# Kernel tuning notes

Measured on AMD Instinct MI355X. Metric: run time of the kernel, lower is better.

## Reference

```python
import jax, jax.numpy as jnp
import numpy as np

E = 256          # embedding_dim
IN = E + 1       # input feature dim (embedding_dim + 1)
B = 128          # batch
N = 1027         # nodes: 1 source + 1024 candidates + 1 destination + 1 depot
REWIRE_P = 0.1


def setup_inputs() -> dict:
    key = jax.random.key(0)
    ks = jax.random.split(key, 16)
    scale = 1.0 / np.sqrt(IN)

    def lin_w(k):
        return jax.random.normal(k, (E, IN), dtype=jnp.float32) * scale

    def lin_b(k):
        return jax.random.normal(k, (E,), dtype=jnp.float32) * scale

    # sparse small-world rewiring weights: nc scalar writes -> one scatter
    nc = int(IN * E * REWIRE_P)  # 6579
    rows = jax.random.randint(ks[10], (nc,), 0, E)
    cols = jax.random.randint(ks[11], (nc,), 0, IN)
    vals = jax.random.normal(ks[12], (nc,), dtype=jnp.float32) * 0.01
    W_rand = jnp.zeros((E, IN), dtype=jnp.float32).at[rows, cols].set(vals)

    return {
        "solutions": jax.random.normal(ks[0], (B, N, IN), dtype=jnp.float32),
        "W_src": lin_w(ks[1]), "b_src": lin_b(ks[2]),
        "W_dst": lin_w(ks[3]), "b_dst": lin_b(ks[4]),
        "W_dep": lin_w(ks[5]), "b_dep": lin_b(ks[6]),
        "W_cand": lin_w(ks[7]), "b_cand": lin_b(ks[8]),
        "W_reg": lin_w(ks[9]), "b_reg": lin_b(ks[13]),
        "W_rand": W_rand,
        "integration_weight": jnp.float32(0.3),
    }


def reference(solutions, W_src, b_src, W_dst, b_dst, W_dep, b_dep,
              W_cand, b_cand, W_reg, b_reg, W_rand, integration_weight):
    # slice node groups: [B,1,IN], [B,N-3,IN], [B,1,IN], [B,1,IN]
    src = solutions[:, :1, :]
    cand = solutions[:, 1:-2, :]
    dst = solutions[:, -2:-1, :]
    dep = solutions[:, -1:, :]

    def lin(x, W, b):
        return jnp.einsum('bnd,ed->bne', x, W) + b

    def sw(x):
        # SmallWorldLayer: regular linear + 0.1 * sparse random matmul
        return lin(x, W_reg, b_reg) + 0.1 * jnp.einsum('bnd,ed->bne', x, W_rand)

    alpha = jax.nn.sigmoid(integration_weight)

    def mix(emb, sw_out):
        return (1.0 - alpha) * emb + alpha * sw_out

    source_emb = mix(lin(src, W_src, b_src), sw(src))
    candidates_emb = mix(lin(cand, W_cand, b_cand), sw(cand))
    destination_emb = mix(lin(dst, W_dst, b_dst), sw(dst))
    depot_emb = mix(lin(dep, W_dep, b_dep), sw(dep))
    return (source_emb, candidates_emb, destination_emb, depot_emb)
```

## Files before the change

kernel.cpp:

```cpp
#include <hip/hip_runtime.h>
#include <hip/hip_bf16.h>

typedef __bf16 bf16x8 __attribute__((ext_vector_type(8)));
typedef __bf16 bf16x4 __attribute__((ext_vector_type(4)));
typedef float  f32x4  __attribute__((ext_vector_type(4)));
typedef float  f32x4u __attribute__((ext_vector_type(4), aligned(4)));

#define BATCH 128
#define NSOL  1027
#define IND   257
#define EMB   256
#define OUT_SRC  0ULL
#define OUT_CAND 32768ULL
#define OUT_DST  33587200ULL
#define OUT_DEP  33619968ULL

#define WFRAG_OFF 0
#define BEFF_OFF  524288
#define W256_OFF  528384

#define XST_B      528
#define X256_OFF_B 16896
#define BUF_B      17024

__global__ __launch_bounds__(256) void swne_prep(
    const float* __restrict__ Wsrc, const float* __restrict__ bsrc,
    const float* __restrict__ Wdst, const float* __restrict__ bdst,
    const float* __restrict__ Wdep, const float* __restrict__ bdep,
    const float* __restrict__ Wcand, const float* __restrict__ bcand,
    const float* __restrict__ Wreg, const float* __restrict__ breg,
    const float* __restrict__ Wrand, const float* __restrict__ iw,
    char* __restrict__ ws)
{
    const float a  = 1.0f / (1.0f + expf(-iw[0]));
    const float ca = 1.0f - a;
    const float sa = 0.1f * a;

    const float* Ws[4] = {Wsrc, Wcand, Wdst, Wdep};
    const float* Bs[4] = {bsrc, bcand, bdst, bdep};

    const int gid = blockIdx.x * 256 + threadIdx.x;
    const int gsz = gridDim.x * 256;

    float* beff = (float*)(ws + BEFF_OFF);
    float* w256 = (float*)(ws + W256_OFF);
    for (int i = gid; i < 4 * EMB; i += gsz) {
        int seg = i >> 8, e = i & 255;
        beff[i] = ca * Bs[seg][e] + a * breg[e];
        int si = e * IND + 256;
        w256[i] = ca * Ws[seg][si] + a * Wreg[si] + sa * Wrand[si];
    }

    __bf16* wfr = (__bf16*)(ws + WFRAG_OFF);
    for (int i = gid; i < 4 * 65536; i += gsz) {
        int seg  = i >> 16;
        int rem  = i & 65535;
        int kk   = rem >> 13;
        int rem2 = rem & 8191;
        int cg   = rem2 >> 9;
        int rem3 = rem2 & 511;
        int l    = rem3 >> 3;
        int j    = rem3 & 7;
        int e = cg * 16 + (l & 15);
        int k = kk * 32 + (l >> 4) * 8 + j;
        int si = e * IND + k;
        wfr[i] = (__bf16)(ca * Ws[seg][si] + a * Wreg[si] + sa * Wrand[si]);
    }
}

__global__ __launch_bounds__(256, 8) void swne_main(const float* __restrict__ sol,
                                                    const char* __restrict__ ws,
                                                    float* __restrict__ out)
{
    __shared__ __align__(16) char smem[BUF_B];
    const int tid = threadIdx.x, bid = blockIdx.x;
    const int lane = tid & 63, wave = tid >> 6;
    const int rl = lane & 15, grp = lane >> 4;

    const float* xbase; size_t xstr; float* obase; int seg;
    if (bid < 4096) {
        const int bb = bid >> 5, t = bid & 31;
        seg   = 1;
        xbase = sol + ((size_t)bb * NSOL + 1 + t * 32) * IND;
        xstr  = IND;
        obase = out + OUT_CAND + ((size_t)bb * 1024 + t * 32) * 256;
    } else {
        const int e = bid - 4096;
        const int s3 = e >> 2, tt = e & 3;
        seg = (s3 == 0) ? 0 : (s3 == 1 ? 2 : 3);
        const int nrow = (s3 == 0) ? 0 : (s3 == 1 ? 1025 : 1026);
        const size_t outb = (s3 == 0) ? OUT_SRC : (s3 == 1 ? OUT_DST : OUT_DEP);
        xbase = sol + ((size_t)(tt * 32) * NSOL + nrow) * IND;
        xstr  = (size_t)NSOL * IND;
        obase = out + outb + (size_t)(tt * 32) * 256;
    }

    #pragma unroll
    for (int rr = 0; rr < 8; ++rr) {
        const int r = wave * 8 + rr;
        f32x4u v = *((const f32x4u*)(xbase + (size_t)r * xstr) + lane);
        bf16x4 h;
        h[0] = (__bf16)v[0]; h[1] = (__bf16)v[1];
        h[2] = (__bf16)v[2]; h[3] = (__bf16)v[3];
        *(bf16x4*)(smem + r * XST_B + lane * 8) = h;
    }
    if (tid < 32)
        *(float*)(smem + X256_OFF_B + tid * 4) = xbase[(size_t)tid * xstr + 256];
    __syncthreads();

    const bf16x8* wfs = (const bf16x8*)(ws + WFRAG_OFF) + (size_t)seg * 8192;
    f32x4 acc[2][4];
    #pragma unroll
    for (int rt = 0; rt < 2; ++rt)
        #pragma unroll
        for (int n = 0; n < 4; ++n) {
            f32x4 z = {0.f, 0.f, 0.f, 0.f};
            acc[rt][n] = z;
        }
    #pragma unroll
    for (int kk = 0; kk < 8; ++kk) {
        bf16x8 a0 = *(const bf16x8*)(smem + rl * XST_B + kk * 64 + grp * 16);
        bf16x8 a1 = *(const bf16x8*)(smem + (16 + rl) * XST_B + kk * 64 + grp * 16);
        #pragma unroll
        for (int n = 0; n < 4; ++n) {
            bf16x8 wv = wfs[(size_t)((kk * 16 + wave * 4 + n) * 64 + lane)];
            acc[0][n] = __builtin_amdgcn_mfma_f32_16x16x32_bf16(wv, a0, acc[0][n], 0, 0, 0);
            acc[1][n] = __builtin_amdgcn_mfma_f32_16x16x32_bf16(wv, a1, acc[1][n], 0, 0, 0);
        }
    }

    const float* bc = (const float*)(ws + BEFF_OFF) + seg * 256;
    const float* wc = (const float*)(ws + W256_OFF) + seg * 256;
    #pragma unroll
    for (int rt = 0; rt < 2; ++rt) {
        const float xl = *(const float*)(smem + X256_OFF_B + (rt * 16 + rl) * 4);
        float* op = obase + (size_t)(rt * 16 + rl) * 256 + wave * 64 + grp * 4;
        #pragma unroll
        for (int n = 0; n < 4; ++n) {
            const int e0 = wave * 64 + n * 16 + grp * 4;
            f32x4 b4 = *(const f32x4*)(bc + e0);
            f32x4 w4 = *(const f32x4*)(wc + e0);
            f32x4 r = acc[rt][n] + xl * w4 + b4;
            *(f32x4*)(op + n * 16) = r;
        }
    }
}

extern "C" void kernel_launch(void* const* d_in, const int* in_sizes, int n_in,
                              void* d_out, int out_size, void* d_ws, size_t ws_size,
                              hipStream_t stream) {
    const float* sol   = (const float*)d_in[0];
    const float* Wsrc  = (const float*)d_in[1];
    const float* bsrc  = (const float*)d_in[2];
    const float* Wdst  = (const float*)d_in[3];
    const float* bdst  = (const float*)d_in[4];
    const float* Wdep  = (const float*)d_in[5];
    const float* bdep  = (const float*)d_in[6];
    const float* Wcand = (const float*)d_in[7];
    const float* bcand = (const float*)d_in[8];
    const float* Wreg  = (const float*)d_in[9];
    const float* breg  = (const float*)d_in[10];
    const float* Wrand = (const float*)d_in[11];
    const float* iw    = (const float*)d_in[12];

    swne_prep<<<512, 256, 0, stream>>>(Wsrc, bsrc, Wdst, bdst, Wdep, bdep,
                                       Wcand, bcand, Wreg, breg, Wrand, iw,
                                       (char*)d_ws);
    swne_main<<<4108, 256, 0, stream>>>(sol, (const char*)d_ws, (float*)d_out);
}
```

Baseline: 73.26 us.

## Use persistent blocks with register-resident weights and a software-pipelined tile loop

The kernel now launches 256 persistent 512-thread blocks, each looping over 16 candidate tiles. Each wave keeps its slice of the candidate weight fragments in registers instead of re-reading them from global memory for every tile. Input rows are prefetched two tiles ahead into registers and written to a 4-slot LDS ring, so loads overlap with MFMA compute. The source, destination and depot rows are handled by the first 12 blocks as tail work. The cost is higher register pressure, fewer resident waves, and possible load imbalance from that tail.

```diff
diff --git a/kernel.cpp b/kernel.cpp
--- a/kernel.cpp
+++ b/kernel.cpp
@@ -68,81 +68,129 @@
     }
 }
 
-__global__ __launch_bounds__(256, 8) void swne_main(const float* __restrict__ sol,
+#define BARRIER() { asm volatile("s_waitcnt lgkmcnt(0)" ::: "memory"); \
+  __builtin_amdgcn_s_barrier(); asm volatile("" ::: "memory"); }
+
+#define ISSUE(xb, xstr, pf, pf256) { \
+  _Pragma("unroll") for (int rr = 0; rr < 4; ++rr) \
+    pf[rr] = *((const f32x4u*)((xb) + (size_t)(wave * 4 + rr) * (xstr)) + lane); \
+  if (tid < 32) pf256 = (xb)[(size_t)tid * (xstr) + 256]; }
+
+#define WRITEB(boff, pf, pf256) { \
+  _Pragma("unroll") for (int rr = 0; rr < 4; ++rr) { \
+    const int r_ = wave * 4 + rr; \
+    bf16x4 h_; \
+    h_[0] = (__bf16)pf[rr][0]; h_[1] = (__bf16)pf[rr][1]; \
+    h_[2] = (__bf16)pf[rr][2]; h_[3] = (__bf16)pf[rr][3]; \
+    *(bf16x4*)(smem + (boff) + r_ * XST_B + lane * 8) = h_; } \
+  if (tid < 32) *(float*)(smem + (boff) + X256_OFF_B + tid * 4) = pf256; }
+
+#define COMPSTORE(boff, obase, W, B4, W4) { \
+  f32x4 acc[2][2]; \
+  _Pragma("unroll") for (int rt = 0; rt < 2; ++rt) \
+    _Pragma("unroll") for (int n = 0; n < 2; ++n) { f32x4 z_ = {0.f,0.f,0.f,0.f}; acc[rt][n] = z_; } \
+  _Pragma("unroll") for (int kk = 0; kk < 8; ++kk) { \
+    bf16x8 a0 = *(const bf16x8*)(smem + (boff) + rl * XST_B + kk * 64 + grp * 16); \
+    bf16x8 a1 = *(const bf16x8*)(smem + (boff) + (16 + rl) * XST_B + kk * 64 + grp * 16); \
+    _Pragma("unroll") for (int n = 0; n < 2; ++n) { \
+      acc[0][n] = __builtin_amdgcn_mfma_f32_16x16x32_bf16(W[kk][n], a0, acc[0][n], 0, 0, 0); \
+      acc[1][n] = __builtin_amdgcn_mfma_f32_16x16x32_bf16(W[kk][n], a1, acc[1][n], 0, 0, 0); } } \
+  _Pragma("unroll") for (int rt = 0; rt < 2; ++rt) { \
+    const float xl = *(const float*)(smem + (boff) + X256_OFF_B + (rt * 16 + rl) * 4); \
+    float* op_ = (obase) + (size_t)(rt * 16 + rl) * 256 + wave * 32 + grp * 4; \
+    _Pragma("unroll") for (int n = 0; n < 2; ++n) { \
+      f32x4 r_ = acc[rt][n] + xl * W4[n] + B4[n]; \
+      *(f32x4*)(op_ + n * 16) = r_; } } }
+
+__device__ __forceinline__ const float* cand_x(const float* sol, int T) {
+    const int bb = T >> 5, t = T & 31;
+    return sol + ((size_t)bb * NSOL + 1 + t * 32) * IND;
+}
+__device__ __forceinline__ float* cand_o(float* out, int T) {
+    const int bb = T >> 5, t = T & 31;
+    return out + OUT_CAND + ((size_t)bb * 1024 + t * 32) * 256;
+}
+
+__global__ __launch_bounds__(512, 1) void swne_main(const float* __restrict__ sol,
                                                     const char* __restrict__ ws,
                                                     float* __restrict__ out)
 {
-    __shared__ __align__(16) char smem[BUF_B];
+    __shared__ __align__(16) char smem[4 * BUF_B];
     const int tid = threadIdx.x, bid = blockIdx.x;
     const int lane = tid & 63, wave = tid >> 6;
     const int rl = lane & 15, grp = lane >> 4;
 
-    const float* xbase; size_t xstr; float* obase; int seg;
-    if (bid < 4096) {
-        const int bb = bid >> 5, t = bid & 31;
-        seg   = 1;
-        xbase = sol + ((size_t)bb * NSOL + 1 + t * 32) * IND;
-        xstr  = IND;
-        obase = out + OUT_CAND + ((size_t)bb * 1024 + t * 32) * 256;
-    } else {
-        const int e = bid - 4096;
-        const int s3 = e >> 2, tt = e & 3;
-        seg = (s3 == 0) ? 0 : (s3 == 1 ? 2 : 3);
+    const bf16x8* wfb = (const bf16x8*)(ws + WFRAG_OFF);
+
+    bf16x8 wreg[8][2];
+    #pragma unroll
+    for (int kk = 0; kk < 8; ++kk)
+        #pragma unroll
+        for (int n = 0; n < 2; ++n)
+            wreg[kk][n] = wfb[(size_t)(((8 + kk) * 16) + (wave * 2 + n)) * 64 + lane];
+
+    const float* bc = (const float*)(ws + BEFF_OFF) + 256;
+    const float* wc = (const float*)(ws + W256_OFF) + 256;
+    f32x4 b4[2], w4[2];
+    #pragma unroll
+    for (int n = 0; n < 2; ++n) {
+        b4[n] = *(const f32x4*)(bc + wave * 32 + n * 16 + grp * 4);
+        w4[n] = *(const f32x4*)(wc + wave * 32 + n * 16 + grp * 4);
+    }
+
+    const int T0 = bid * 16;
+    f32x4 pfA[4], pfB[4]; float pA256 = 0.f, pB256 = 0.f;
+
+    ISSUE(cand_x(sol, T0 + 0), IND, pfA, pA256);
+    ISSUE(cand_x(sol, T0 + 1), IND, pfB, pB256);
+    WRITEB(0 * BUF_B, pfA, pA256);
+    WRITEB(1 * BUF_B, pfB, pB256);
+    ISSUE(cand_x(sol, T0 + 2), IND, pfA, pA256);
+    ISSUE(cand_x(sol, T0 + 3), IND, pfB, pB256);
+    BARRIER();
+
+    for (int k = 0; k < 16; k += 2) {
+        COMPSTORE((size_t)(k & 3) * BUF_B, cand_o(out, T0 + k), wreg, b4, w4);
+        if (k + 2 < 16) {
+            WRITEB((size_t)((k + 2) & 3) * BUF_B, pfA, pA256);
+            if (k + 4 < 16) ISSUE(cand_x(sol, T0 + k + 4), IND, pfA, pA256);
+        }
+        COMPSTORE((size_t)((k + 1) & 3) * BUF_B, cand_o(out, T0 + k + 1), wreg, b4, w4);
+        if (k + 3 < 16) {
+            WRITEB((size_t)((k + 3) & 3) * BUF_B, pfB, pB256);
+            if (k + 5 < 16) ISSUE(cand_x(sol, T0 + k + 5), IND, pfB, pB256);
+        }
+        BARRIER();
+    }
+
+    if (bid < 12) {
+        const int s3 = bid >> 2, tt = bid & 3;
+        const int seg = (s3 == 0) ? 0 : (s3 == 1 ? 2 : 3);
         const int nrow = (s3 == 0) ? 0 : (s3 == 1 ? 1025 : 1026);
         const size_t outb = (s3 == 0) ? OUT_SRC : (s3 == 1 ? OUT_DST : OUT_DEP);
-        xbase = sol + ((size_t)(tt * 32) * NSOL + nrow) * IND;
-        xstr  = (size_t)NSOL * IND;
-        obase = out + outb + (size_t)(tt * 32) * 256;
-    }
-
-    #pragma unroll
-    for (int rr = 0; rr < 8; ++rr) {
-        const int r = wave * 8 + rr;
-        f32x4u v = *((const f32x4u*)(xbase + (size_t)r * xstr) + lane);
-        bf16x4 h;
-        h[0] = (__bf16)v[0]; h[1] = (__bf16)v[1];
-        h[2] = (__bf16)v[2]; h[3] = (__bf16)v[3];
-        *(bf16x4*)(smem + r * XST_B + lane * 8) = h;
-    }
-    if (tid < 32)
-        *(float*)(smem + X256_OFF_B + tid * 4) = xbase[(size_t)tid * xstr + 256];
-    __syncthreads();
-
-    const bf16x8* wfs = (const bf16x8*)(ws + WFRAG_OFF) + (size_t)seg * 8192;
-    f32x4 acc[2][4];
-    #pragma unroll
-    for (int rt = 0; rt < 2; ++rt)
+        const float* xe = sol + ((size_t)(tt * 32) * NSOL + nrow) * IND;
+        float* oe = out + outb + (size_t)(tt * 32) * 256;
+        const size_t xstrE = (size_t)NSOL * IND;
+
+        bf16x8 wregE[8][2];
         #pragma unroll
-        for (int n = 0; n < 4; ++n) {
-            f32x4 z = {0.f, 0.f, 0.f, 0.f};
-            acc[rt][n] = z;
+        for (int kk = 0; kk < 8; ++kk)
+            #pragma unroll
+            for (int n = 0; n < 2; ++n)
+                wregE[kk][n] = wfb[(size_t)(((seg * 8 + kk) * 16) + (wave * 2 + n)) * 64 + lane];
+        const float* bcE = (const float*)(ws + BEFF_OFF) + seg * 256;
+        const float* wcE = (const float*)(ws + W256_OFF) + seg * 256;
+        f32x4 b4E[2], w4E[2];
+        #pragma unroll
+        for (int n = 0; n < 2; ++n) {
+            b4E[n] = *(const f32x4*)(bcE + wave * 32 + n * 16 + grp * 4);
+            w4E[n] = *(const f32x4*)(wcE + wave * 32 + n * 16 + grp * 4);
         }
-    #pragma unroll
-    for (int kk = 0; kk < 8; ++kk) {
-        bf16x8 a0 = *(const bf16x8*)(smem + rl * XST_B + kk * 64 + grp * 16);
-        bf16x8 a1 = *(const bf16x8*)(smem + (16 + rl) * XST_B + kk * 64 + grp * 16);
-        #pragma unroll
-        for (int n = 0; n < 4; ++n) {
-            bf16x8 wv = wfs[(size_t)((kk * 16 + wave * 4 + n) * 64 + lane)];
-            acc[0][n] = __builtin_amdgcn_mfma_f32_16x16x32_bf16(wv, a0, acc[0][n], 0, 0, 0);
-            acc[1][n] = __builtin_amdgcn_mfma_f32_16x16x32_bf16(wv, a1, acc[1][n], 0, 0, 0);
-        }
-    }
-
-    const float* bc = (const float*)(ws + BEFF_OFF) + seg * 256;
-    const float* wc = (const float*)(ws + W256_OFF) + seg * 256;
-    #pragma unroll
-    for (int rt = 0; rt < 2; ++rt) {
-        const float xl = *(const float*)(smem + X256_OFF_B + (rt * 16 + rl) * 4);
-        float* op = obase + (size_t)(rt * 16 + rl) * 256 + wave * 64 + grp * 4;
-        #pragma unroll
-        for (int n = 0; n < 4; ++n) {
-            const int e0 = wave * 64 + n * 16 + grp * 4;
-            f32x4 b4 = *(const f32x4*)(bc + e0);
-            f32x4 w4 = *(const f32x4*)(wc + e0);
-            f32x4 r = acc[rt][n] + xl * w4 + b4;
-            *(f32x4*)(op + n * 16) = r;
-        }
+
+        ISSUE(xe, xstrE, pfA, pA256);
+        WRITEB(0, pfA, pA256);
+        BARRIER();
+        COMPSTORE(0, oe, wregE, b4E, w4E);
     }
 }
 
@@ -166,5 +214,5 @@
     swne_prep<<<512, 256, 0, stream>>>(Wsrc, bsrc, Wdst, bdst, Wdep, bdep,
                                        Wcand, bcand, Wreg, breg, Wrand, iw,
                                        (char*)d_ws);
-    swne_main<<<4108, 256, 0, stream>>>(sol, (const char*)d_ws, (float*)d_out);
-}
+    swne_main<<<256, 512, 0, stream>>>(sol, (const char*)d_ws, (float*)d_out);
+}
```

After: 67.16 us. -8.3%, faster.
